# Optimization experiments

Measured on AMD Instinct MI355X. Metric: run time of the kernel, lower is better.

Reference implementation:

```python
import jax, jax.numpy as jnp
import numpy as np


def _grid_pull_linear_zero(input, grid):
    """Trilinear grid_pull, bound='zero', extrapolate=False, prefilter=False.
    input: (B, C, Nx, Ny, Nz); grid: (B, 3, Xo, Yo, Zo) voxel coords.
    """
    g = jnp.moveaxis(grid, 1, -1)                      # (B, Xo, Yo, Zo, 3)
    B, C, Nx, Ny, Nz = input.shape
    sizes = jnp.array([Nx, Ny, Nz], dtype=jnp.int32)
    f = jnp.floor(g)
    w = g - f                                          # fractional part in [0,1)
    f = f.astype(jnp.int32)
    inp_flat = input.reshape(B, C, -1)                 # (B, C, Nx*Ny*Nz)
    out = jnp.zeros((B, C, g.shape[1] * g.shape[2] * g.shape[3]), input.dtype)
    for dx in (0, 1):
        for dy in (0, 1):
            for dz in (0, 1):
                off = jnp.array([dx, dy, dz], dtype=jnp.int32)
                idx = f + off                          # (B,Xo,Yo,Zo,3)
                # zero bound: out-of-range taps contribute nothing
                valid = jnp.all((idx >= 0) & (idx < sizes), axis=-1)
                wc = jnp.prod(jnp.where(off == 1, w, 1.0 - w), axis=-1)
                ic = jnp.clip(idx, 0, sizes - 1)
                flat = (ic[..., 0] * Ny + ic[..., 1]) * Nz + ic[..., 2]
                vals = jnp.take_along_axis(inp_flat, flat.reshape(B, 1, -1), axis=2)
                out = out + vals * (wc * valid).reshape(B, 1, -1).astype(input.dtype)
    out = out.reshape(B, C, g.shape[1], g.shape[2], g.shape[3])
    # extrapolate=False: zero voxels sampled outside the field of view
    inb = jnp.all((g >= 0) & (g <= (sizes - 1).astype(g.dtype)), axis=-1)
    return out * inb[:, None].astype(out.dtype)


def setup_inputs() -> dict:
    key = jax.random.key(0)
    k1, k2 = jax.random.split(key)
    B, C, N = 2, 2, 128
    input = jax.random.normal(k1, (B, C, N, N, N), dtype=jnp.float32)
    # voxel coordinates spanning the full input volume [0, N-1]
    grid = jax.random.uniform(k2, (B, 3, N, N, N), dtype=jnp.float32) * (N - 1)
    return {"input": input, "grid": grid}


def reference(input, grid):
    return _grid_pull_linear_zero(input, grid)
```

## Files before the change

### kernel.cpp

```cpp
#include <hip/hip_runtime.h>


#define NDIM 128
#define NV   (128 * 128 * 128)

typedef float f4 __attribute__((ext_vector_type(4)));
typedef float f2 __attribute__((ext_vector_type(2)));

__global__ __launch_bounds__(256) void repack_kernel(
    const float* __restrict__ input, float* __restrict__ pk)
{
    const int t  = blockIdx.x * blockDim.x + threadIdx.x;
    const int v4 = t << 2;
    const int b  = v4 >> 21;
    const int v  = v4 & (NV - 1);
    const float* base = input + (size_t)b * 2 * NV;
    const f4 a = *reinterpret_cast<const f4*>(base + v);
    const f4 c = *reinterpret_cast<const f4*>(base + NV + v);
    f4 w0, w1;
    w0.x = a.x; w0.y = c.x; w0.z = a.y; w0.w = c.y;
    w1.x = a.z; w1.y = c.z; w1.z = a.w; w1.w = c.w;
    float* o = pk + (size_t)b * 2 * NV + 2 * v;
    *reinterpret_cast<f4*>(o)     = w0;
    *reinterpret_cast<f4*>(o + 4) = w1;
}

__global__ __launch_bounds__(256) void grid_pull_packed_kernel(
    const float* __restrict__ pk,
    const float* __restrict__ grid,
    float* __restrict__ out)
{
    const int t  = blockIdx.x * blockDim.x + threadIdx.x;
    const int p4 = t << 2;
    const int b  = p4 >> 21;
    const int s  = p4 & (NV - 1);

    const float* gbase = grid + (size_t)b * 3 * NV;
    const f4 gx = __builtin_nontemporal_load(reinterpret_cast<const f4*>(gbase + s));
    const f4 gy = __builtin_nontemporal_load(reinterpret_cast<const f4*>(gbase + NV + s));
    const f4 gz = __builtin_nontemporal_load(reinterpret_cast<const f4*>(gbase + 2 * NV + s));

    const float* p = pk + (size_t)b * 2 * NV;

    int sbase[4];
#pragma unroll
    for (int k = 0; k < 4; ++k) {
        const int ix = (int)floorf(gx[k]);
        const int iy = (int)floorf(gy[k]);
        const int iz = (int)floorf(gz[k]);
        const bool interior = ((unsigned)ix < (unsigned)(NDIM - 1)) &
                              ((unsigned)iy < (unsigned)(NDIM - 1)) &
                              ((unsigned)iz < (unsigned)(NDIM - 1));
        const int base = (ix << 15) + (iy << 8) + (iz << 1);
        sbase[k] = interior ? base : 0;
    }

    const int off[8] = {0, 2, 256, 258, 32768, 32770, 33024, 33026};
    f2 tv[4][8];
#pragma unroll
    for (int k = 0; k < 4; ++k) {
#pragma unroll
        for (int j = 0; j < 8; ++j) {
            tv[k][j] = *reinterpret_cast<const f2*>(p + sbase[k] + off[j]);
        }
    }

    f4 o0, o1;
#pragma unroll
    for (int k = 0; k < 4; ++k) {
        const float x = gx[k], y = gy[k], z = gz[k];
        const float fx = floorf(x), fy = floorf(y), fz = floorf(z);
        const float wx = x - fx, wy = y - fy, wz = z - fz;
        const int ix = (int)fx, iy = (int)fy, iz = (int)fz;

        const bool inb = (x >= 0.0f) & (x <= (float)(NDIM - 1)) &
                         (y >= 0.0f) & (y <= (float)(NDIM - 1)) &
                         (z >= 0.0f) & (z <= (float)(NDIM - 1));
        const bool interior = inb &
                              ((unsigned)ix < (unsigned)(NDIM - 1)) &
                              ((unsigned)iy < (unsigned)(NDIM - 1)) &
                              ((unsigned)iz < (unsigned)(NDIM - 1));

        const float wx0 = 1.0f - wx, wy0 = 1.0f - wy, wz0 = 1.0f - wz;
        const float w00 = wx0 * wy0, w01 = wx0 * wy;
        const float w10 = wx  * wy0, w11 = wx  * wy;
        float wt[8];
        wt[0] = w00 * wz0; wt[1] = w00 * wz;
        wt[2] = w01 * wz0; wt[3] = w01 * wz;
        wt[4] = w10 * wz0; wt[5] = w10 * wz;
        wt[6] = w11 * wz0; wt[7] = w11 * wz;

        float acc0 = 0.0f, acc1 = 0.0f;
#pragma unroll
        for (int j = 0; j < 8; ++j) {
            acc0 = fmaf(tv[k][j].x, wt[j], acc0);
            acc1 = fmaf(tv[k][j].y, wt[j], acc1);
        }
        const float m = interior ? 1.0f : 0.0f;
        acc0 *= m; acc1 *= m;

        if (inb & !interior) {
            acc0 = 0.0f; acc1 = 0.0f;
            for (int dx = 0; dx < 2; ++dx) {
                const int X = ix + dx;
                if ((unsigned)X >= (unsigned)NDIM) continue;
                const float wxd = dx ? wx : wx0;
                for (int dy = 0; dy < 2; ++dy) {
                    const int Y = iy + dy;
                    if ((unsigned)Y >= (unsigned)NDIM) continue;
                    const float wyd = dy ? wy : wy0;
                    for (int dz = 0; dz < 2; ++dz) {
                        const int Z = iz + dz;
                        if ((unsigned)Z >= (unsigned)NDIM) continue;
                        const float wzd = dz ? wz : wz0;
                        const float w = wxd * wyd * wzd;
                        const f2 v = *reinterpret_cast<const f2*>(
                            p + (X << 15) + (Y << 8) + (Z << 1));
                        acc0 = fmaf(v.x, w, acc0);
                        acc1 = fmaf(v.y, w, acc1);
                    }
                }
            }
        }
        o0[k] = acc0;
        o1[k] = acc1;
    }

    float* obase = out + (size_t)b * 2 * NV + s;
    __builtin_nontemporal_store(o0, reinterpret_cast<f4*>(obase));
    __builtin_nontemporal_store(o1, reinterpret_cast<f4*>(obase + NV));
}

__global__ __launch_bounds__(256) void grid_pull_direct_kernel(
    const float* __restrict__ input,
    const float* __restrict__ grid,
    float* __restrict__ out)
{
    const int t  = blockIdx.x * blockDim.x + threadIdx.x;
    const int p4 = t << 2;
    const int b  = p4 >> 21;
    const int s  = p4 & (NV - 1);

    const float* gbase = grid + (size_t)b * 3 * NV;
    const f4 gx = *reinterpret_cast<const f4*>(gbase + s);
    const f4 gy = *reinterpret_cast<const f4*>(gbase + NV + s);
    const f4 gz = *reinterpret_cast<const f4*>(gbase + 2 * NV + s);
    const float* in0 = input + (size_t)b * 2 * NV;
    const float* in1 = in0 + NV;

    f4 o0, o1;
#pragma unroll
    for (int k = 0; k < 4; ++k) {
        const float x = gx[k], y = gy[k], z = gz[k];
        const float fx = floorf(x), fy = floorf(y), fz = floorf(z);
        const float wx = x - fx, wy = y - fy, wz = z - fz;
        const int ix = (int)fx, iy = (int)fy, iz = (int)fz;
        const bool inb = (x >= 0.0f) & (x <= (float)(NDIM - 1)) &
                         (y >= 0.0f) & (y <= (float)(NDIM - 1)) &
                         (z >= 0.0f) & (z <= (float)(NDIM - 1));
        float acc0 = 0.0f, acc1 = 0.0f;
        if (inb) {
            for (int dx = 0; dx < 2; ++dx) {
                const int X = ix + dx;
                if ((unsigned)X >= (unsigned)NDIM) continue;
                const float wxd = dx ? wx : 1.0f - wx;
                for (int dy = 0; dy < 2; ++dy) {
                    const int Y = iy + dy;
                    if ((unsigned)Y >= (unsigned)NDIM) continue;
                    const float wyd = dy ? wy : 1.0f - wy;
                    for (int dz = 0; dz < 2; ++dz) {
                        const int Z = iz + dz;
                        if ((unsigned)Z >= (unsigned)NDIM) continue;
                        const float w = wxd * wyd * (dz ? wz : 1.0f - wz);
                        const int idx = (X << 14) + (Y << 7) + Z;
                        acc0 = fmaf(in0[idx], w, acc0);
                        acc1 = fmaf(in1[idx], w, acc1);
                    }
                }
            }
        }
        o0[k] = acc0;
        o1[k] = acc1;
    }
    float* obase = out + (size_t)b * 2 * NV + s;
    *reinterpret_cast<f4*>(obase)      = o0;
    *reinterpret_cast<f4*>(obase + NV) = o1;
}

extern "C" void kernel_launch(void* const* d_in, const int* in_sizes, int n_in,
                              void* d_out, int out_size, void* d_ws, size_t ws_size,
                              hipStream_t stream) {
    const float* input = (const float*)d_in[0];
    const float* grid  = (const float*)d_in[1];
    float* out         = (float*)d_out;

    const int threads_total = (2 * NV) / 4;
    const int block = 256;
    const int ngrid = threads_total / block;
    const size_t need = (size_t)2 * 2 * NV * sizeof(float);

    if (ws_size >= need) {
        float* pk = (float*)d_ws;
        repack_kernel<<<ngrid, block, 0, stream>>>(input, pk);
        grid_pull_packed_kernel<<<ngrid, block, 0, stream>>>(pk, grid, out);
    } else {
        grid_pull_direct_kernel<<<ngrid, block, 0, stream>>>(input, grid, out);
    }
}
```

Before: 345.6 us.

## Bin sample points by x-slab before trilinear gather to improve cache locality

Adds a multi-pass path. First, grid points are scattered into 16 bins, one per batch and 16-plane x-slab, using shared-memory counters plus global atomic cursors, and each point's destination index is recorded. A gather kernel then interpolates each bin's points straight from the unpacked input, so each block's random taps fall in a small slab that should stay in L2, and an unpermute kernel writes results back in original order. The aim is to replace scattered, cache-missing gathers over the whole volume with slab-local ones. The cost is extra traffic for the records, results and position arrays, three extra launches, and a much larger workspace requirement; the older packed and direct paths are kept as fallbacks.

```diff
diff --git a/kernel.cpp b/kernel.cpp
--- a/kernel.cpp
+++ b/kernel.cpp
@@ -3,9 +3,175 @@
 
 #define NDIM 128
 #define NV   (128 * 128 * 128)
+#define NPTS (2 * NV)
+#define NBINS 16
+#define CAP  270336
+#define NBLK 4096
 
 typedef float f4 __attribute__((ext_vector_type(4)));
 typedef float f2 __attribute__((ext_vector_type(2)));
+typedef int   i4 __attribute__((ext_vector_type(4)));
+
+__device__ __forceinline__ int bin_of(float x, int b) {
+    int ix = (int)floorf(x);
+    int slab = min(max(ix, 0), NDIM - 1) >> 4;
+    return (b << 3) + slab;
+}
+
+__global__ void p0_zero(int* __restrict__ cursor) {
+    if (threadIdx.x < 64) cursor[threadIdx.x] = 0;
+}
+
+__global__ __launch_bounds__(256) void p3_scatter(
+    const float* __restrict__ grid,
+    f4* __restrict__ rec,
+    int* __restrict__ pos,
+    int* __restrict__ cursor)
+{
+    __shared__ int lcnt[NBINS];
+    __shared__ int lbase[NBINS];
+    const int t  = blockIdx.x * blockDim.x + threadIdx.x;
+    const int p4 = t << 2;
+    const int b  = p4 >> 21;
+    const int s  = p4 & (NV - 1);
+
+    if (threadIdx.x < NBINS) lcnt[threadIdx.x] = 0;
+    __syncthreads();
+
+    const float* gbase = grid + (size_t)b * 3 * NV;
+    const f4 gx = __builtin_nontemporal_load(reinterpret_cast<const f4*>(gbase + s));
+    const f4 gy = __builtin_nontemporal_load(reinterpret_cast<const f4*>(gbase + NV + s));
+    const f4 gz = __builtin_nontemporal_load(reinterpret_cast<const f4*>(gbase + 2 * NV + s));
+
+    int mybin[4], myrank[4];
+#pragma unroll
+    for (int k = 0; k < 4; ++k) {
+        mybin[k]  = bin_of(gx[k], b);
+        myrank[k] = atomicAdd(&lcnt[mybin[k]], 1);
+    }
+    __syncthreads();
+    if (threadIdx.x < NBINS)
+        lbase[threadIdx.x] = atomicAdd(&cursor[threadIdx.x], lcnt[threadIdx.x]);
+    __syncthreads();
+
+    i4 dvec;
+#pragma unroll
+    for (int k = 0; k < 4; ++k) {
+        const int d = mybin[k] * CAP + lbase[mybin[k]] + myrank[k];
+        f4 r;
+        r.x = gx[k]; r.y = gy[k]; r.z = gz[k];
+        r.w = __int_as_float(p4 + k);
+        __builtin_nontemporal_store(r, &rec[d]);
+        dvec[k] = d;
+    }
+    __builtin_nontemporal_store(dvec, reinterpret_cast<i4*>(pos + p4));
+}
+
+__global__ __launch_bounds__(256) void p4_gather(
+    const float* __restrict__ input,
+    const f4* __restrict__ rec,
+    f2* __restrict__ res,
+    const int* __restrict__ cursor)
+{
+    const int bid = blockIdx.x;
+    const int bin   = (bid < (NBLK / 2)) ? (bid & 7) : 8 + (bid & 7);
+    const int chunk = (bid & (NBLK / 2 - 1)) >> 3;
+    const int cnt   = cursor[bin];
+    const int b     = bin >> 3;
+    const int seg   = bin * CAP;
+    const float* vin = input + (size_t)b * 2 * NV;
+
+    for (int i = chunk * 1024 + (threadIdx.x << 2); i < cnt; i += 256 * 1024) {
+#pragma unroll
+        for (int k = 0; k < 4; ++k) {
+            if (i + k >= cnt) break;
+            const int d = seg + i + k;
+            const f4 r = __builtin_nontemporal_load(&rec[d]);
+            const float x = r.x, y = r.y, z = r.z;
+
+            const float fx = floorf(x), fy = floorf(y), fz = floorf(z);
+            const float wx = x - fx, wy = y - fy, wz = z - fz;
+            const int ix = (int)fx, iy = (int)fy, iz = (int)fz;
+
+            const bool inb = (x >= 0.0f) & (x <= (float)(NDIM - 1)) &
+                             (y >= 0.0f) & (y <= (float)(NDIM - 1)) &
+                             (z >= 0.0f) & (z <= (float)(NDIM - 1));
+            const bool interior = inb &
+                                  ((unsigned)ix < (unsigned)(NDIM - 1)) &
+                                  ((unsigned)iy < (unsigned)(NDIM - 1)) &
+                                  ((unsigned)iz < (unsigned)(NDIM - 1));
+            float acc0 = 0.0f, acc1 = 0.0f;
+            if (interior) {
+                const int base = (ix << 14) + (iy << 7) + iz;
+                const float wx0 = 1.0f - wx, wy0 = 1.0f - wy, wz0 = 1.0f - wz;
+                const float w00 = wx0 * wy0, w01 = wx0 * wy;
+                const float w10 = wx  * wy0, w11 = wx  * wy;
+                const f2 a00 = *reinterpret_cast<const f2*>(vin + base);
+                const f2 a01 = *reinterpret_cast<const f2*>(vin + base + 128);
+                const f2 a10 = *reinterpret_cast<const f2*>(vin + base + 16384);
+                const f2 a11 = *reinterpret_cast<const f2*>(vin + base + 16512);
+                const f2 c00 = *reinterpret_cast<const f2*>(vin + NV + base);
+                const f2 c01 = *reinterpret_cast<const f2*>(vin + NV + base + 128);
+                const f2 c10 = *reinterpret_cast<const f2*>(vin + NV + base + 16384);
+                const f2 c11 = *reinterpret_cast<const f2*>(vin + NV + base + 16512);
+                const float z00 = fmaf(a00.y, wz, a00.x * wz0);
+                const float z01 = fmaf(a01.y, wz, a01.x * wz0);
+                const float z10 = fmaf(a10.y, wz, a10.x * wz0);
+                const float z11 = fmaf(a11.y, wz, a11.x * wz0);
+                acc0 = fmaf(z11, w11, fmaf(z10, w10, fmaf(z01, w01, z00 * w00)));
+                const float u00 = fmaf(c00.y, wz, c00.x * wz0);
+                const float u01 = fmaf(c01.y, wz, c01.x * wz0);
+                const float u10 = fmaf(c10.y, wz, c10.x * wz0);
+                const float u11 = fmaf(c11.y, wz, c11.x * wz0);
+                acc1 = fmaf(u11, w11, fmaf(u10, w10, fmaf(u01, w01, u00 * w00)));
+            } else if (inb) {
+                for (int dx = 0; dx < 2; ++dx) {
+                    const int X = ix + dx;
+                    if ((unsigned)X >= (unsigned)NDIM) continue;
+                    const float wxd = dx ? wx : 1.0f - wx;
+                    for (int dy = 0; dy < 2; ++dy) {
+                        const int Y = iy + dy;
+                        if ((unsigned)Y >= (unsigned)NDIM) continue;
+                        const float wyd = dy ? wy : 1.0f - wy;
+                        for (int dz = 0; dz < 2; ++dz) {
+                            const int Z = iz + dz;
+                            if ((unsigned)Z >= (unsigned)NDIM) continue;
+                            const float w = wxd * wyd * (dz ? wz : 1.0f - wz);
+                            const int idx = (X << 14) + (Y << 7) + Z;
+                            acc0 = fmaf(vin[idx], w, acc0);
+                            acc1 = fmaf(vin[NV + idx], w, acc1);
+                        }
+                    }
+                }
+            }
+            f2 o; o.x = acc0; o.y = acc1;
+            res[d] = o;
+        }
+    }
+}
+
+__global__ __launch_bounds__(256) void p5_unpermute(
+    const f2* __restrict__ res,
+    const int* __restrict__ pos,
+    float* __restrict__ out)
+{
+    const int t  = blockIdx.x * blockDim.x + threadIdx.x;
+    const int p4 = t << 2;
+    const int b  = p4 >> 21;
+    const int s  = p4 & (NV - 1);
+
+    const i4 dd = __builtin_nontemporal_load(reinterpret_cast<const i4*>(pos + p4));
+    const f2 r0 = res[dd.x];
+    const f2 r1 = res[dd.y];
+    const f2 r2 = res[dd.z];
+    const f2 r3 = res[dd.w];
+    f4 o0, o1;
+    o0.x = r0.x; o0.y = r1.x; o0.z = r2.x; o0.w = r3.x;
+    o1.x = r0.y; o1.y = r1.y; o1.z = r2.y; o1.w = r3.y;
+    float* obase = out + (size_t)b * 2 * NV + s;
+    __builtin_nontemporal_store(o0, reinterpret_cast<f4*>(obase));
+    __builtin_nontemporal_store(o1, reinterpret_cast<f4*>(obase + NV));
+}
 
 __global__ __launch_bounds__(256) void repack_kernel(
     const float* __restrict__ input, float* __restrict__ pk)
@@ -34,36 +200,11 @@
     const int p4 = t << 2;
     const int b  = p4 >> 21;
     const int s  = p4 & (NV - 1);
-
     const float* gbase = grid + (size_t)b * 3 * NV;
-    const f4 gx = __builtin_nontemporal_load(reinterpret_cast<const f4*>(gbase + s));
-    const f4 gy = __builtin_nontemporal_load(reinterpret_cast<const f4*>(gbase + NV + s));
-    const f4 gz = __builtin_nontemporal_load(reinterpret_cast<const f4*>(gbase + 2 * NV + s));
-
+    const f4 gx = *reinterpret_cast<const f4*>(gbase + s);
+    const f4 gy = *reinterpret_cast<const f4*>(gbase + NV + s);
+    const f4 gz = *reinterpret_cast<const f4*>(gbase + 2 * NV + s);
     const float* p = pk + (size_t)b * 2 * NV;
-
-    int sbase[4];
-#pragma unroll
-    for (int k = 0; k < 4; ++k) {
-        const int ix = (int)floorf(gx[k]);
-        const int iy = (int)floorf(gy[k]);
-        const int iz = (int)floorf(gz[k]);
-        const bool interior = ((unsigned)ix < (unsigned)(NDIM - 1)) &
-                              ((unsigned)iy < (unsigned)(NDIM - 1)) &
-                              ((unsigned)iz < (unsigned)(NDIM - 1));
-        const int base = (ix << 15) + (iy << 8) + (iz << 1);
-        sbase[k] = interior ? base : 0;
-    }
-
-    const int off[8] = {0, 2, 256, 258, 32768, 32770, 33024, 33026};
-    f2 tv[4][8];
-#pragma unroll
-    for (int k = 0; k < 4; ++k) {
-#pragma unroll
-        for (int j = 0; j < 8; ++j) {
-            tv[k][j] = *reinterpret_cast<const f2*>(p + sbase[k] + off[j]);
-        }
-    }
 
     f4 o0, o1;
 #pragma unroll
@@ -72,48 +213,23 @@
         const float fx = floorf(x), fy = floorf(y), fz = floorf(z);
         const float wx = x - fx, wy = y - fy, wz = z - fz;
         const int ix = (int)fx, iy = (int)fy, iz = (int)fz;
-
         const bool inb = (x >= 0.0f) & (x <= (float)(NDIM - 1)) &
                          (y >= 0.0f) & (y <= (float)(NDIM - 1)) &
                          (z >= 0.0f) & (z <= (float)(NDIM - 1));
-        const bool interior = inb &
-                              ((unsigned)ix < (unsigned)(NDIM - 1)) &
-                              ((unsigned)iy < (unsigned)(NDIM - 1)) &
-                              ((unsigned)iz < (unsigned)(NDIM - 1));
-
-        const float wx0 = 1.0f - wx, wy0 = 1.0f - wy, wz0 = 1.0f - wz;
-        const float w00 = wx0 * wy0, w01 = wx0 * wy;
-        const float w10 = wx  * wy0, w11 = wx  * wy;
-        float wt[8];
-        wt[0] = w00 * wz0; wt[1] = w00 * wz;
-        wt[2] = w01 * wz0; wt[3] = w01 * wz;
-        wt[4] = w10 * wz0; wt[5] = w10 * wz;
-        wt[6] = w11 * wz0; wt[7] = w11 * wz;
-
         float acc0 = 0.0f, acc1 = 0.0f;
-#pragma unroll
-        for (int j = 0; j < 8; ++j) {
-            acc0 = fmaf(tv[k][j].x, wt[j], acc0);
-            acc1 = fmaf(tv[k][j].y, wt[j], acc1);
-        }
-        const float m = interior ? 1.0f : 0.0f;
-        acc0 *= m; acc1 *= m;
-
-        if (inb & !interior) {
-            acc0 = 0.0f; acc1 = 0.0f;
+        if (inb) {
             for (int dx = 0; dx < 2; ++dx) {
                 const int X = ix + dx;
                 if ((unsigned)X >= (unsigned)NDIM) continue;
-                const float wxd = dx ? wx : wx0;
+                const float wxd = dx ? wx : 1.0f - wx;
                 for (int dy = 0; dy < 2; ++dy) {
                     const int Y = iy + dy;
                     if ((unsigned)Y >= (unsigned)NDIM) continue;
-                    const float wyd = dy ? wy : wy0;
+                    const float wyd = dy ? wy : 1.0f - wy;
                     for (int dz = 0; dz < 2; ++dz) {
                         const int Z = iz + dz;
                         if ((unsigned)Z >= (unsigned)NDIM) continue;
-                        const float wzd = dz ? wz : wz0;
-                        const float w = wxd * wyd * wzd;
+                        const float w = wxd * wyd * (dz ? wz : 1.0f - wz);
                         const f2 v = *reinterpret_cast<const f2*>(
                             p + (X << 15) + (Y << 8) + (Z << 1));
                         acc0 = fmaf(v.x, w, acc0);
@@ -122,13 +238,11 @@
                 }
             }
         }
-        o0[k] = acc0;
-        o1[k] = acc1;
-    }
-
+        o0[k] = acc0; o1[k] = acc1;
+    }
     float* obase = out + (size_t)b * 2 * NV + s;
-    __builtin_nontemporal_store(o0, reinterpret_cast<f4*>(obase));
-    __builtin_nontemporal_store(o1, reinterpret_cast<f4*>(obase + NV));
+    *reinterpret_cast<f4*>(obase)      = o0;
+    *reinterpret_cast<f4*>(obase + NV) = o1;
 }
 
 __global__ __launch_bounds__(256) void grid_pull_direct_kernel(
@@ -140,14 +254,12 @@
     const int p4 = t << 2;
     const int b  = p4 >> 21;
     const int s  = p4 & (NV - 1);
-
     const float* gbase = grid + (size_t)b * 3 * NV;
     const f4 gx = *reinterpret_cast<const f4*>(gbase + s);
     const f4 gy = *reinterpret_cast<const f4*>(gbase + NV + s);
     const f4 gz = *reinterpret_cast<const f4*>(gbase + 2 * NV + s);
     const float* in0 = input + (size_t)b * 2 * NV;
     const float* in1 = in0 + NV;
-
     f4 o0, o1;
 #pragma unroll
     for (int k = 0; k < 4; ++k) {
@@ -179,8 +291,7 @@
                 }
             }
         }
-        o0[k] = acc0;
-        o1[k] = acc1;
+        o0[k] = acc0; o1[k] = acc1;
     }
     float* obase = out + (size_t)b * 2 * NV + s;
     *reinterpret_cast<f4*>(obase)      = o0;
@@ -194,16 +305,31 @@
     const float* grid  = (const float*)d_in[1];
     float* out         = (float*)d_out;
 
-    const int threads_total = (2 * NV) / 4;
+    const size_t rec_bytes  = (size_t)NBINS * CAP * sizeof(f4);
+    const size_t pos_bytes  = (size_t)NPTS * sizeof(int);
+    const size_t res_bytes  = (size_t)NBINS * CAP * sizeof(f2);
+    const size_t cur_bytes  = 256;
+    const size_t need_bin   = rec_bytes + pos_bytes + res_bytes + cur_bytes;
+    const size_t need_pack  = (size_t)2 * 2 * NV * sizeof(float);
+
     const int block = 256;
-    const int ngrid = threads_total / block;
-    const size_t need = (size_t)2 * 2 * NV * sizeof(float);
-
-    if (ws_size >= need) {
+
+    if (ws_size >= need_bin) {
+        char* w = (char*)d_ws;
+        f4*  rec    = (f4*)w;
+        int* pos    = (int*)(w + rec_bytes);
+        f2*  res    = (f2*)(w + rec_bytes + pos_bytes);
+        int* cursor = (int*)(w + rec_bytes + pos_bytes + res_bytes);
+
+        p0_zero<<<1, 64, 0, stream>>>(cursor);
+        p3_scatter<<<NBLK, block, 0, stream>>>(grid, rec, pos, cursor);
+        p4_gather<<<NBLK, block, 0, stream>>>(input, rec, res, cursor);
+        p5_unpermute<<<NBLK, block, 0, stream>>>(res, pos, out);
+    } else if (ws_size >= need_pack) {
         float* pk = (float*)d_ws;
-        repack_kernel<<<ngrid, block, 0, stream>>>(input, pk);
-        grid_pull_packed_kernel<<<ngrid, block, 0, stream>>>(pk, grid, out);
+        repack_kernel<<<NBLK, block, 0, stream>>>(input, pk);
+        grid_pull_packed_kernel<<<NBLK, block, 0, stream>>>(pk, grid, out);
     } else {
-        grid_pull_direct_kernel<<<ngrid, block, 0, stream>>>(input, grid, out);
-    }
-}
+        grid_pull_direct_kernel<<<NBLK, block, 0, stream>>>(input, grid, out);
+    }
+}
```

Result: no change. 343.1 us (-0.7%).
